# Optimization experiments

Hardware: AMD Instinct MI355X
Metric: run time of the kernel (lower is better)

Reference implementation:

```python
import jax, jax.numpy as jnp
import numpy as np

BLOCK = 128
FP8_MAX = 448.0  # max representable value of float8_e4m3fn
F8 = jnp.float8_e4m3fn


def setup_inputs() -> dict:
    key = jax.random.key(0)
    k1, k2, k3 = jax.random.split(key, 3)
    M, K, N = 4096, 7168, 16384
    x = jax.random.normal(k1, (M, K), jnp.float32)
    w = jax.random.normal(k2, (N, K), jnp.float32)  # raw weight; cast to fp8 in reference to simulate stored fp8
    w_scale = jax.random.uniform(k3, (N // BLOCK, K // BLOCK), jnp.float32, 0.5, 1.5)
    return {"x": x, "w": w, "w_scale": w_scale, "block_size": BLOCK}


def act_quant(x, b):
    M, K = x.shape
    xb = x.reshape(M, K // b, b)
    s = jnp.max(jnp.abs(xb), axis=-1) / FP8_MAX  # [M, K//b]
    xq = (xb / s[..., None]).astype(F8).astype(jnp.float32).reshape(M, K)
    return xq, s


def reference(x, w, w_scale, block_size):
    b = block_size
    # simulate fp8-stored weight (element_size == 1 branch)
    w8 = w.astype(F8).astype(jnp.float32)  # [N, K]
    # fp8_gemm: y[m,n] = sum_k xq[m,k]*w8[n,k]*xs[m,kb]*ws[nb,kb]
    # scales factor per-element, so dequantize both operands then one dense GEMM
    xq, xs = act_quant(x, b)
    x_dq = xq * jnp.repeat(xs, b, axis=1)                         # [M, K]
    w_dq = w8 * jnp.repeat(jnp.repeat(w_scale, b, axis=0), b, axis=1)  # [N, K]
    return x_dq @ w_dq.T  # [M, N], no bias (bias=False)
```

## Files before the change

### kernel.cpp

```cpp
#include <hip/hip_runtime.h>
#include <hip/hip_bf16.h>
#include <hip/hip_fp8.h>

typedef __attribute__((ext_vector_type(8))) short short8;
typedef __attribute__((ext_vector_type(4))) float f32x4;

#define AS1 __attribute__((address_space(1)))
#define AS3 __attribute__((address_space(3)))

static constexpr int Mdim = 4096;
static constexpr int Kdim = 7168;
static constexpr int Ndim = 16384;
static constexpr float FP8_MAX = 448.0f;

#define BARRIER() do { asm volatile("" ::: "memory"); \
                       __builtin_amdgcn_s_barrier();  \
                       asm volatile("" ::: "memory"); } while (0)

#define MFMA_BF16 __builtin_amdgcn_mfma_f32_16x16x32_bf16

__global__ __launch_bounds__(256) void quant_x_kernel(
    const float* __restrict__ x, __hip_bfloat16* __restrict__ xdq)
{
    constexpr int NBLK = Mdim * (Kdim / 128);
    const int lane = threadIdx.x & 63;
    const int wid  = (blockIdx.x * 256 + threadIdx.x) >> 6;
    const int nw   = (gridDim.x * 256) >> 6;

    for (int b = wid; b < NBLK; b += nw) {
        size_t base = (size_t)b * 128 + lane * 2;
        float2 v = *reinterpret_cast<const float2*>(x + base);
        float amax = fmaxf(fabsf(v.x), fabsf(v.y));
#pragma unroll
        for (int off = 32; off > 0; off >>= 1)
            amax = fmaxf(amax, __shfl_xor(amax, off));
        float s = amax * (1.0f / FP8_MAX);
        float q0 = 0.0f, q1 = 0.0f;
        if (s > 0.0f) {
            q0 = (float)__hip_fp8_e4m3(v.x / s) * s;
            q1 = (float)__hip_fp8_e4m3(v.y / s) * s;
        }
        __hip_bfloat162 o;
        o.x = __float2bfloat16(q0);
        o.y = __float2bfloat16(q1);
        *reinterpret_cast<__hip_bfloat162*>(xdq + base) = o;
    }
}

__global__ __launch_bounds__(256) void quant_w_kernel(
    const float* __restrict__ w, const float* __restrict__ ws,
    __hip_bfloat16* __restrict__ wdq)
{
    constexpr size_t NCHUNK = (size_t)Ndim * Kdim / 8;
    constexpr int CPR = Kdim / 8;
    constexpr int KB  = Kdim / 128;

    size_t idx    = (size_t)blockIdx.x * 256 + threadIdx.x;
    size_t stride = (size_t)gridDim.x * 256;

    for (size_t c = idx; c < NCHUNK; c += stride) {
        int n  = (int)(c / CPR);
        int kc = (int)(c - (size_t)n * CPR);
        int k  = kc * 8;
        float s = ws[(n >> 7) * KB + (k >> 7)];
        const float* src = w + (size_t)n * Kdim + k;
        float4 v0 = *reinterpret_cast<const float4*>(src);
        float4 v1 = *reinterpret_cast<const float4*>(src + 4);

        __hip_bfloat16 h[8];
        h[0] = __float2bfloat16((float)__hip_fp8_e4m3(v0.x) * s);
        h[1] = __float2bfloat16((float)__hip_fp8_e4m3(v0.y) * s);
        h[2] = __float2bfloat16((float)__hip_fp8_e4m3(v0.z) * s);
        h[3] = __float2bfloat16((float)__hip_fp8_e4m3(v0.w) * s);
        h[4] = __float2bfloat16((float)__hip_fp8_e4m3(v1.x) * s);
        h[5] = __float2bfloat16((float)__hip_fp8_e4m3(v1.y) * s);
        h[6] = __float2bfloat16((float)__hip_fp8_e4m3(v1.z) * s);
        h[7] = __float2bfloat16((float)__hip_fp8_e4m3(v1.w) * s);
        *reinterpret_cast<short8*>(wdq + (size_t)n * Kdim + k) =
            *reinterpret_cast<short8*>(h);
    }
}

constexpr int BM = 256, BN = 256, BK = 64;
constexpr int NT  = Kdim / BK;
constexpr int NBN = Ndim / BN;
constexpr int NWG = (Mdim / BM) * NBN;

__global__ __launch_bounds__(512, 2) void gemm256_kernel(
    const __hip_bfloat16* __restrict__ Ag,
    const __hip_bfloat16* __restrict__ Bg,
    float* __restrict__ C)
{
    extern __shared__ char smem[];

    const int tid  = threadIdx.x;
    const int w    = tid >> 6;
    const int lane = tid & 63;
    const int wr   = w >> 2;
    const int wc   = w & 3;
    const int lr   = lane & 15;
    const int lk   = lane >> 4;

    int bid = (int)blockIdx.x;
    int swz = (bid & 7) * (NWG >> 3) + (bid >> 3);
    const int bm = (swz / NBN) * BM;
    const int bn = (swz % NBN) * BN;

    const int sw   = (lr & 7) << 4;
    const int col0 = (lk * 16) ^ sw;
    const int col1 = (64 + lk * 16) ^ sw;
    const int bRow = (wc & 1) * 64;

    int rowL[2], colB[2], ldsW[2];
#pragma unroll
    for (int q = 0; q < 2; ++q) {
        int chp = (w * 2 + q) * 64 + lane;
        rowL[q] = chp >> 3;
        colB[q] = ((chp & 7) ^ (rowL[q] & 7)) * 16;
        ldsW[q] = (w * 2 + q) * 1024;
    }

    auto stage = [&](int j) {
        if (j >= 4 * NT) return;
        const int T    = j >> 2;
        const int r    = j & 3;
        const int isA  = r >> 1;
        const int half = r & 1;
        const int regByte = (T & 1) * 65536 + (isA ? 0 : 32768) + half * 16384;
        const __hip_bfloat16* base = isA ? Ag : Bg;
        const int rowBase = (isA ? bm : bn) + half * 128;
#pragma unroll
        for (int q = 0; q < 2; ++q) {
            const char* g = (const char*)(base + (size_t)(rowBase + rowL[q]) * Kdim + T * 64)
                            + colB[q];
            __builtin_amdgcn_global_load_lds((const AS1 void*)g,
                                             (AS3 void*)(smem + regByte + ldsW[q]),
                                             16, 0, 0);
        }
    };

    for (int j = 0; j < 6; ++j) stage(j);
    asm volatile("s_waitcnt vmcnt(4)" ::: "memory");
    BARRIER();

    f32x4 acc[8][4] = {};

    for (int t = 0; t < NT; ++t) {
        const int buf = t & 1;
        const char* aB = smem + buf * 65536 + wr * 16384;
        const char* bB = smem + buf * 65536 + 32768 + (wc >> 1) * 16384;
        short8 a0[4][2], a1[4][2], b0[2][2], b1[2][2];

#pragma unroll
        for (int m = 0; m < 4; ++m) {
            const char* p = aB + (m * 16 + lr) * 128;
            a0[m][0] = *(const short8*)(p + col0);
            a0[m][1] = *(const short8*)(p + col1);
        }
#pragma unroll
        for (int n = 0; n < 2; ++n) {
            const char* p = bB + (bRow + n * 16 + lr) * 128;
            b0[n][0] = *(const short8*)(p + col0);
            b0[n][1] = *(const short8*)(p + col1);
        }
        stage(4 * t + 6);
        BARRIER();
        __builtin_amdgcn_s_setprio(1);
#pragma unroll
        for (int m = 0; m < 4; ++m)
#pragma unroll
            for (int n = 0; n < 2; ++n) {
                acc[m][n] = MFMA_BF16(a0[m][0], b0[n][0], acc[m][n], 0, 0, 0);
                acc[m][n] = MFMA_BF16(a0[m][1], b0[n][1], acc[m][n], 0, 0, 0);
            }
        __builtin_amdgcn_s_setprio(0);
        BARRIER();

#pragma unroll
        for (int n = 0; n < 2; ++n) {
            const char* p = bB + (bRow + (n + 2) * 16 + lr) * 128;
            b1[n][0] = *(const short8*)(p + col0);
            b1[n][1] = *(const short8*)(p + col1);
        }
        stage(4 * t + 7);
        BARRIER();
        __builtin_amdgcn_s_setprio(1);
#pragma unroll
        for (int m = 0; m < 4; ++m)
#pragma unroll
            for (int n = 0; n < 2; ++n) {
                acc[m][n + 2] = MFMA_BF16(a0[m][0], b1[n][0], acc[m][n + 2], 0, 0, 0);
                acc[m][n + 2] = MFMA_BF16(a0[m][1], b1[n][1], acc[m][n + 2], 0, 0, 0);
            }
        __builtin_amdgcn_s_setprio(0);
        BARRIER();

#pragma unroll
        for (int m = 0; m < 4; ++m) {
            const char* p = aB + ((m + 4) * 16 + lr) * 128;
            a1[m][0] = *(const short8*)(p + col0);
            a1[m][1] = *(const short8*)(p + col1);
        }
        stage(4 * t + 8);
        BARRIER();
        __builtin_amdgcn_s_setprio(1);
#pragma unroll
        for (int m = 0; m < 4; ++m)
#pragma unroll
            for (int n = 0; n < 2; ++n) {
                acc[m + 4][n] = MFMA_BF16(a1[m][0], b0[n][0], acc[m + 4][n], 0, 0, 0);
                acc[m + 4][n] = MFMA_BF16(a1[m][1], b0[n][1], acc[m + 4][n], 0, 0, 0);
            }
        __builtin_amdgcn_s_setprio(0);
        BARRIER();

        stage(4 * t + 9);
        BARRIER();
        __builtin_amdgcn_s_setprio(1);
#pragma unroll
        for (int m = 0; m < 4; ++m)
#pragma unroll
            for (int n = 0; n < 2; ++n) {
                acc[m + 4][n + 2] = MFMA_BF16(a1[m][0], b1[n][0], acc[m + 4][n + 2], 0, 0, 0);
                acc[m + 4][n + 2] = MFMA_BF16(a1[m][1], b1[n][1], acc[m + 4][n + 2], 0, 0, 0);
            }
        __builtin_amdgcn_s_setprio(0);
        if (t < NT - 2) { asm volatile("s_waitcnt vmcnt(4)" ::: "memory"); }
        else            { asm volatile("s_waitcnt vmcnt(0)" ::: "memory"); }
        BARRIER();
    }

#pragma unroll
    for (int m = 0; m < 8; ++m) {
#pragma unroll
        for (int n = 0; n < 4; ++n) {
            const int row0 = bm + wr * 128 + m * 16 + lk * 4;
            const int col  = bn + wc * 64 + n * 16 + lr;
#pragma unroll
            for (int j = 0; j < 4; ++j)
                C[(size_t)(row0 + j) * Ndim + col] = acc[m][n][j];
        }
    }
}

extern "C" void kernel_launch(void* const* d_in, const int* in_sizes, int n_in,
                              void* d_out, int out_size, void* d_ws, size_t ws_size,
                              hipStream_t stream) {
    const float* x  = (const float*)d_in[0];
    const float* w  = (const float*)d_in[1];
    const float* ws = (const float*)d_in[2];

    __hip_bfloat16* xdq = (__hip_bfloat16*)d_ws;
    __hip_bfloat16* wdq = xdq + (size_t)Mdim * Kdim;

    quant_x_kernel<<<2048, 256, 0, stream>>>(x, xdq);
    quant_w_kernel<<<4096, 256, 0, stream>>>(w, ws, wdq);

    hipFuncSetAttribute((const void*)gemm256_kernel,
                        hipFuncAttributeMaxDynamicSharedMemorySize, 131072);
    gemm256_kernel<<<NWG, 512, 131072, stream>>>(xdq, wdq, (float*)d_out);
}
```

Measured before the change: 981.2 us.

## Switch GEMM inner loop to 32x32x16 bf16 MFMA with 32-row fragments

Replaces the 16x16x32 bf16 MFMA tiles with 32x32x16 MFMAs, so each wave now holds 4x2 f32x16 accumulators instead of 8x4 f32x4. LDS fragment loads and the swizzled column offsets are reorganised for 32-row operands, and the epilogue store mapping is rewritten for the 32x32 output layout. Global load address arithmetic is also precomputed into per-thread byte offsets to cut address math in the staging lambda. The larger MFMA does more work per instruction and needs fewer LDS reads per FLOP, at the cost of different register pressure and possibly different LDS bank behaviour.

```diff
diff --git a/kernel.cpp b/kernel.cpp
--- a/kernel.cpp
+++ b/kernel.cpp
@@ -4,6 +4,7 @@
 
 typedef __attribute__((ext_vector_type(8))) short short8;
 typedef __attribute__((ext_vector_type(4))) float f32x4;
+typedef __attribute__((ext_vector_type(16))) float f32x16;
 
 #define AS1 __attribute__((address_space(1)))
 #define AS3 __attribute__((address_space(3)))
@@ -17,7 +18,7 @@
                        __builtin_amdgcn_s_barrier();  \
                        asm volatile("" ::: "memory"); } while (0)
 
-#define MFMA_BF16 __builtin_amdgcn_mfma_f32_16x16x32_bf16
+#define MFMA32 __builtin_amdgcn_mfma_f32_32x32x16_bf16
 
 __global__ __launch_bounds__(256) void quant_x_kernel(
     const float* __restrict__ x, __hip_bfloat16* __restrict__ xdq)
@@ -85,6 +86,7 @@
 constexpr int NT  = Kdim / BK;
 constexpr int NBN = Ndim / BN;
 constexpr int NWG = (Mdim / BM) * NBN;
+constexpr int K2  = Kdim * 2;
 
 __global__ __launch_bounds__(512, 2) void gemm256_kernel(
     const __hip_bfloat16* __restrict__ Ag,
@@ -98,27 +100,32 @@
     const int lane = tid & 63;
     const int wr   = w >> 2;
     const int wc   = w & 3;
-    const int lr   = lane & 15;
-    const int lk   = lane >> 4;
+    const int l31  = lane & 31;
+    const int hi16 = (lane >> 5) * 16;
 
     int bid = (int)blockIdx.x;
     int swz = (bid & 7) * (NWG >> 3) + (bid >> 3);
     const int bm = (swz / NBN) * BM;
     const int bn = (swz % NBN) * BN;
 
-    const int sw   = (lr & 7) << 4;
-    const int col0 = (lk * 16) ^ sw;
-    const int col1 = (64 + lk * 16) ^ sw;
+    const int sw = (lane & 7) << 4;
+    int colks[4];
+#pragma unroll
+    for (int ks = 0; ks < 4; ++ks) colks[ks] = (ks * 32 + hi16) ^ sw;
     const int bRow = (wc & 1) * 64;
 
-    int rowL[2], colB[2], ldsW[2];
+    size_t offG[2];
+    int    ldsW[2];
 #pragma unroll
     for (int q = 0; q < 2; ++q) {
-        int chp = (w * 2 + q) * 64 + lane;
-        rowL[q] = chp >> 3;
-        colB[q] = ((chp & 7) ^ (rowL[q] & 7)) * 16;
-        ldsW[q] = (w * 2 + q) * 1024;
-    }
+        int chp  = (w * 2 + q) * 64 + lane;
+        int row  = chp >> 3;
+        int colb = ((chp & 7) ^ (row & 7)) * 16;
+        offG[q]  = (size_t)row * K2 + colb;
+        ldsW[q]  = (w * 2 + q) * 1024;
+    }
+    const char* Ab = (const char*)Ag + (size_t)bm * K2;
+    const char* Bb = (const char*)Bg + (size_t)bn * K2;
 
     auto stage = [&](int j) {
         if (j >= 4 * NT) return;
@@ -127,90 +134,83 @@
         const int isA  = r >> 1;
         const int half = r & 1;
         const int regByte = (T & 1) * 65536 + (isA ? 0 : 32768) + half * 16384;
-        const __hip_bfloat16* base = isA ? Ag : Bg;
-        const int rowBase = (isA ? bm : bn) + half * 128;
-#pragma unroll
-        for (int q = 0; q < 2; ++q) {
-            const char* g = (const char*)(base + (size_t)(rowBase + rowL[q]) * Kdim + T * 64)
-                            + colB[q];
-            __builtin_amdgcn_global_load_lds((const AS1 void*)g,
+        const char* g = (isA ? Ab : Bb) + (size_t)half * (128 * (size_t)K2)
+                        + (size_t)T * 128;
+#pragma unroll
+        for (int q = 0; q < 2; ++q)
+            __builtin_amdgcn_global_load_lds((const AS1 void*)(g + offG[q]),
                                              (AS3 void*)(smem + regByte + ldsW[q]),
                                              16, 0, 0);
-        }
     };
 
     for (int j = 0; j < 6; ++j) stage(j);
     asm volatile("s_waitcnt vmcnt(4)" ::: "memory");
     BARRIER();
 
-    f32x4 acc[8][4] = {};
+    f32x16 acc[4][2] = {};
 
     for (int t = 0; t < NT; ++t) {
         const int buf = t & 1;
         const char* aB = smem + buf * 65536 + wr * 16384;
         const char* bB = smem + buf * 65536 + 32768 + (wc >> 1) * 16384;
-        short8 a0[4][2], a1[4][2], b0[2][2], b1[2][2];
-
-#pragma unroll
-        for (int m = 0; m < 4; ++m) {
-            const char* p = aB + (m * 16 + lr) * 128;
-            a0[m][0] = *(const short8*)(p + col0);
-            a0[m][1] = *(const short8*)(p + col1);
-        }
-#pragma unroll
-        for (int n = 0; n < 2; ++n) {
-            const char* p = bB + (bRow + n * 16 + lr) * 128;
-            b0[n][0] = *(const short8*)(p + col0);
-            b0[n][1] = *(const short8*)(p + col1);
+        short8 a0[2][4], a1[2][4], b0[4], b1[4];
+
+#pragma unroll
+        for (int m = 0; m < 2; ++m) {
+            const char* p = aB + (m * 32 + l31) * 128;
+#pragma unroll
+            for (int ks = 0; ks < 4; ++ks)
+                a0[m][ks] = *(const short8*)(p + colks[ks]);
+        }
+        {
+            const char* p = bB + (bRow + l31) * 128;
+#pragma unroll
+            for (int ks = 0; ks < 4; ++ks)
+                b0[ks] = *(const short8*)(p + colks[ks]);
         }
         stage(4 * t + 6);
         BARRIER();
         __builtin_amdgcn_s_setprio(1);
 #pragma unroll
-        for (int m = 0; m < 4; ++m)
-#pragma unroll
-            for (int n = 0; n < 2; ++n) {
-                acc[m][n] = MFMA_BF16(a0[m][0], b0[n][0], acc[m][n], 0, 0, 0);
-                acc[m][n] = MFMA_BF16(a0[m][1], b0[n][1], acc[m][n], 0, 0, 0);
-            }
-        __builtin_amdgcn_s_setprio(0);
-        BARRIER();
-
-#pragma unroll
-        for (int n = 0; n < 2; ++n) {
-            const char* p = bB + (bRow + (n + 2) * 16 + lr) * 128;
-            b1[n][0] = *(const short8*)(p + col0);
-            b1[n][1] = *(const short8*)(p + col1);
+        for (int m = 0; m < 2; ++m)
+#pragma unroll
+            for (int ks = 0; ks < 4; ++ks)
+                acc[m][0] = MFMA32(a0[m][ks], b0[ks], acc[m][0], 0, 0, 0);
+        __builtin_amdgcn_s_setprio(0);
+        BARRIER();
+
+        {
+            const char* p = bB + (bRow + 32 + l31) * 128;
+#pragma unroll
+            for (int ks = 0; ks < 4; ++ks)
+                b1[ks] = *(const short8*)(p + colks[ks]);
         }
         stage(4 * t + 7);
         BARRIER();
         __builtin_amdgcn_s_setprio(1);
 #pragma unroll
-        for (int m = 0; m < 4; ++m)
-#pragma unroll
-            for (int n = 0; n < 2; ++n) {
-                acc[m][n + 2] = MFMA_BF16(a0[m][0], b1[n][0], acc[m][n + 2], 0, 0, 0);
-                acc[m][n + 2] = MFMA_BF16(a0[m][1], b1[n][1], acc[m][n + 2], 0, 0, 0);
-            }
-        __builtin_amdgcn_s_setprio(0);
-        BARRIER();
-
-#pragma unroll
-        for (int m = 0; m < 4; ++m) {
-            const char* p = aB + ((m + 4) * 16 + lr) * 128;
-            a1[m][0] = *(const short8*)(p + col0);
-            a1[m][1] = *(const short8*)(p + col1);
+        for (int m = 0; m < 2; ++m)
+#pragma unroll
+            for (int ks = 0; ks < 4; ++ks)
+                acc[m][1] = MFMA32(a0[m][ks], b1[ks], acc[m][1], 0, 0, 0);
+        __builtin_amdgcn_s_setprio(0);
+        BARRIER();
+
+#pragma unroll
+        for (int m = 0; m < 2; ++m) {
+            const char* p = aB + ((m + 2) * 32 + l31) * 128;
+#pragma unroll
+            for (int ks = 0; ks < 4; ++ks)
+                a1[m][ks] = *(const short8*)(p + colks[ks]);
         }
         stage(4 * t + 8);
         BARRIER();
         __builtin_amdgcn_s_setprio(1);
 #pragma unroll
-        for (int m = 0; m < 4; ++m)
-#pragma unroll
-            for (int n = 0; n < 2; ++n) {
-                acc[m + 4][n] = MFMA_BF16(a1[m][0], b0[n][0], acc[m + 4][n], 0, 0, 0);
-                acc[m + 4][n] = MFMA_BF16(a1[m][1], b0[n][1], acc[m + 4][n], 0, 0, 0);
-            }
+        for (int m = 0; m < 2; ++m)
+#pragma unroll
+            for (int ks = 0; ks < 4; ++ks)
+                acc[m + 2][0] = MFMA32(a1[m][ks], b0[ks], acc[m + 2][0], 0, 0, 0);
         __builtin_amdgcn_s_setprio(0);
         BARRIER();
 
@@ -218,27 +218,29 @@
         BARRIER();
         __builtin_amdgcn_s_setprio(1);
 #pragma unroll
-        for (int m = 0; m < 4; ++m)
-#pragma unroll
-            for (int n = 0; n < 2; ++n) {
-                acc[m + 4][n + 2] = MFMA_BF16(a1[m][0], b1[n][0], acc[m + 4][n + 2], 0, 0, 0);
-                acc[m + 4][n + 2] = MFMA_BF16(a1[m][1], b1[n][1], acc[m + 4][n + 2], 0, 0, 0);
-            }
+        for (int m = 0; m < 2; ++m)
+#pragma unroll
+            for (int ks = 0; ks < 4; ++ks)
+                acc[m + 2][1] = MFMA32(a1[m][ks], b1[ks], acc[m + 2][1], 0, 0, 0);
         __builtin_amdgcn_s_setprio(0);
         if (t < NT - 2) { asm volatile("s_waitcnt vmcnt(4)" ::: "memory"); }
         else            { asm volatile("s_waitcnt vmcnt(0)" ::: "memory"); }
         BARRIER();
     }
 
-#pragma unroll
-    for (int m = 0; m < 8; ++m) {
-#pragma unroll
-        for (int n = 0; n < 4; ++n) {
-            const int row0 = bm + wr * 128 + m * 16 + lk * 4;
-            const int col  = bn + wc * 64 + n * 16 + lr;
-#pragma unroll
-            for (int j = 0; j < 4; ++j)
-                C[(size_t)(row0 + j) * Ndim + col] = acc[m][n][j];
+    const int rsub = 4 * (lane >> 5);
+#pragma unroll
+    for (int m = 0; m < 4; ++m) {
+#pragma unroll
+        for (int n = 0; n < 2; ++n) {
+            const f32x16 v   = acc[m][n];
+            const int    col = bn + wc * 64 + n * 32 + l31;
+            const int    rb  = bm + wr * 128 + m * 32 + rsub;
+#pragma unroll
+            for (int reg = 0; reg < 16; ++reg) {
+                const int row = rb + (reg & 3) + 8 * (reg >> 2);
+                C[(size_t)row * Ndim + col] = v[reg];
+            }
         }
     }
 }
```

Result: slower. 1.096 ms (+11.7%).
